# Performance work log

Hardware: AMD Instinct MI355X
Metric: run time of the kernel (lower is better)

## Reference

```python
import jax, jax.numpy as jnp
import numpy as np

VERY_NEG = -1e30

H = 768           # hidden_size
A_DIM = 768       # attention_dim_size
N_TREE = 40000    # num_tree_nodes (embed_init vocab)
N_CODES = 10000   # number of leaf codes (rows of leaves_list)
MAX_ANC = 8       # max ancestors per code
B, V, M = 16, 32, 48  # batch, visits, codes per visit
OUT = 512         # classifier output_size


def setup_inputs() -> dict:
    key = jax.random.key(0)
    ks = jax.random.split(key, 12)
    leaves_list = jax.random.randint(ks[0], (N_CODES, MAX_ANC), 0, N_TREE)
    ancestors_list = jax.random.randint(ks[1], (N_CODES, MAX_ANC), 0, N_TREE)
    masks = (jax.random.uniform(ks[2], (N_CODES, MAX_ANC)) > 0.3).astype(jnp.float32)
    masks = masks.at[:, 0].set(1.0)  # ensure at least one valid ancestor
    input_ids = jax.random.randint(ks[3], (B, V, M), 0, N_CODES + 1)  # 0 is padding row
    code_mask = (jax.random.uniform(ks[4], (B, V, M)) > 0.2).astype(jnp.float32)
    code_mask = code_mask.at[:, :, 0].set(1.0)
    s = 1.0 / np.sqrt(H)
    embed_table = jax.random.normal(ks[5], (N_TREE, H), dtype=jnp.float32) * s
    w1 = jax.random.normal(ks[6], (2 * H, A_DIM), dtype=jnp.float32) * (1.0 / np.sqrt(2 * H))
    b1 = jnp.zeros((A_DIM,), dtype=jnp.float32)
    w2 = jax.random.normal(ks[7], (A_DIM, 1), dtype=jnp.float32) * (1.0 / np.sqrt(A_DIM))
    b2 = jnp.zeros((1,), dtype=jnp.float32)
    wc = jax.random.normal(ks[8], (H, OUT), dtype=jnp.float32) * s
    bc = jnp.zeros((OUT,), dtype=jnp.float32)
    return {
        "embed_table": embed_table, "w1": w1, "b1": b1, "w2": w2, "b2": b2,
        "wc": wc, "bc": bc, "masks": masks, "code_mask": code_mask,
        "leaves_list": leaves_list, "ancestors_list": ancestors_list,
        "input_ids": input_ids,
    }


def reference(embed_table, w1, b1, w2, b2, wc, bc, masks, code_mask,
              leaves_list, ancestors_list, input_ids):
    # --- DAGAttention2D over ancestor axis ---
    leaves = embed_table[leaves_list]        # [N, A, H]
    ancestors = embed_table[ancestors_list]  # [N, A, H]
    m = masks[:, :, None]                    # [N, A, 1]
    x = jnp.concatenate([leaves * m, ancestors * m], axis=-1)  # [N, A, 2H]
    x = jax.nn.relu(jnp.einsum('nah,hd->nad', x, w1) + b1)
    x = jnp.einsum('nad,do->nao', x, w2) + b2                  # [N, A, 1]
    x = x + (1.0 - m) * VERY_NEG
    attn = jax.nn.softmax(x, axis=1)                           # softmax over ancestors
    dag_emb = (attn * ancestors * m).sum(axis=1)               # [N, H]
    # --- dict_matrix with padding row 0, embedding lookup ---
    dict_matrix = jnp.concatenate([jnp.zeros((1, dag_emb.shape[1]), dag_emb.dtype), dag_emb], axis=0)
    emb = dict_matrix[input_ids]             # [B, V, M, H]
    cm = code_mask[..., None]
    pooled = (emb * cm).sum(axis=2) / jnp.clip(cm.sum(axis=2), 1.0, None)  # [B, V, H]
    # --- Classifier (dropout inactive at eval, activation=None) ---
    out = jnp.einsum('bvh,ho->bvo', pooled, wc) + bc           # [B, V, OUT]
    return out
```

## Files before the change

### kernel.cpp

```cpp
#include <hip/hip_runtime.h>
#include <stdint.h>

typedef unsigned short u16;
typedef __bf16 bfx8 __attribute__((ext_vector_type(8)));
typedef float f32x4 __attribute__((ext_vector_type(4)));

#define HD 768
#define NTREE 40000
#define NCODES 10000
#define GNN 1536
#define OUTD 512
#define NBV 512
#define VNEG (-1e30f)
#define TB 4

#define BM 256
#define BN 256
#define BK 64
#define NKT (HD / BK)
#define NMT ((NTREE + BM - 1) / BM)
#define NNT (GNN / BN)
#define GRID (NMT * NNT)
#define Q8 (GRID / 8)
#define R8 (GRID % 8)

#define WAITV(n) asm volatile("s_waitcnt vmcnt(" #n ")" ::: "memory")
#define LGKM(n)  asm volatile("s_waitcnt lgkmcnt(" #n ")" ::: "memory")

__device__ __forceinline__ float bf2f(u16 u) {
  union { uint32_t i; float f; } v; v.i = ((uint32_t)u) << 16; return v.f;
}
__device__ __forceinline__ u16 f2bf(float f) {
  union { float fl; uint32_t i; } v; v.fl = f;
  uint32_t u = v.i;
  u += 0x7FFFu + ((u >> 16) & 1u);
  return (u16)(u >> 16);
}

#define NBLK_CONV 30000
__global__ void k_prep(const float* __restrict__ E, u16* __restrict__ Ebf,
                       const float* __restrict__ w1, u16* __restrict__ Bt) {
  const int bid = blockIdx.x, tid = threadIdx.x;
  if (bid < NBLK_CONV) {
    const int i = bid * 256 + tid;
    float4 v = ((const float4*)E)[i];
    ushort4 r;
    r.x = f2bf(v.x); r.y = f2bf(v.y); r.z = f2bf(v.z); r.w = f2bf(v.w);
    ((ushort4*)Ebf)[i] = r;
  } else {
    const int idx = (bid - NBLK_CONV) * 256 + tid;
    if (idx < GNN * HD) {
      const int n = idx / HD, k = idx % HD;
      const int srow = k + ((n >= HD) ? HD : 0);
      const int scol = (n >= HD) ? (n - HD) : n;
      Bt[idx] = f2bf(w1[(size_t)srow * HD + scol]);
    }
  }
}

__global__ __launch_bounds__(512, 2) void k_gemm(const u16* __restrict__ A,
                                                 const u16* __restrict__ B,
                                                 u16* __restrict__ C) {
  __shared__ u16 lds[65536];

  const int tid    = threadIdx.x;
  const int lane   = tid & 63;
  const int wv     = tid >> 6;
  const int wr     = wv >> 2;
  const int wc     = wv & 3;
  const int lane15 = lane & 15;
  const int g      = lane >> 4;

  const int orig = blockIdx.x;
  const int xcd = orig & 7, lin = orig >> 3;
  const int wg = (xcd < R8 ? xcd * (Q8 + 1) : R8 * (Q8 + 1) + (xcd - R8) * Q8) + lin;
  const int mt = wg / NNT, nt = wg % NNT;
  const int tm = mt * BM, tn = nt * BN;

  uint32_t aOff[2][2], bOff[2][2];
#pragma unroll
  for (int u = 0; u < 2; ++u) {
    const int o    = u * 8192 + tid * 16;
    const int rloc = o >> 7;
    const int c    = ((o >> 4) & 7) ^ (rloc & 7);
#pragma unroll
    for (int h = 0; h < 2; ++h) {
      int ra = tm + h * 128 + rloc; if (ra > NTREE - 1) ra = NTREE - 1;
      aOff[u][h] = (uint32_t)ra * HD + c * 8;
      bOff[u][h] = (uint32_t)(tn + h * 128 + rloc) * HD + c * 8;
    }
  }

#define STAGE_A(MH, NB, TT) do {                                               \
    _Pragma("unroll") for (int u = 0; u < 2; ++u)                              \
      __builtin_amdgcn_global_load_lds(                                        \
        (const __attribute__((address_space(1))) void*)(A + aOff[u][MH] + (TT) * BK), \
        (__attribute__((address_space(3))) void*)((char*)lds + (NB) * 32768 +  \
            (MH) * 16384 + u * 8192 + tid * 16),                               \
        16, 0, 0);                                                             \
  } while (0)

#define STAGE_B(NH, NB, TT) do {                                               \
    _Pragma("unroll") for (int u = 0; u < 2; ++u)                              \
      __builtin_amdgcn_global_load_lds(                                        \
        (const __attribute__((address_space(1))) void*)(B + bOff[u][NH] + (TT) * BK), \
        (__attribute__((address_space(3))) void*)((char*)lds + 65536 +         \
            (NB) * 32768 + (NH) * 16384 + u * 8192 + tid * 16),                \
        16, 0, 0);                                                             \
  } while (0)

  f32x4 acc[4][4][2];
#pragma unroll
  for (int q = 0; q < 4; ++q)
#pragma unroll
    for (int i = 0; i < 4; ++i)
#pragma unroll
      for (int j = 0; j < 2; ++j) acc[q][i][j] = (f32x4){0.f, 0.f, 0.f, 0.f};

  int colz[2];
  colz[0] = ((0 * 4 + g) ^ (lane15 & 7)) * 8;
  colz[1] = ((1 * 4 + g) ^ (lane15 & 7)) * 8;
  const int aLane = wr * 4096 + lane15 * 64;
  const int bLane = wc * 2048 + lane15 * 64;

  bfx8 aF[4][2], bF[2][2];

#define READ_A(MH, BA) do {                                                    \
    _Pragma("unroll") for (int mf = 0; mf < 4; ++mf)                           \
      _Pragma("unroll") for (int ks = 0; ks < 2; ++ks)                         \
        aF[mf][ks] = *(const bfx8*)&lds[(BA) + (MH) * 8192 + aLane +           \
                                        mf * 1024 + colz[ks]];                 \
  } while (0)

#define READ_B(NH, BB) do {                                                    \
    _Pragma("unroll") for (int nf = 0; nf < 2; ++nf)                           \
      _Pragma("unroll") for (int ks = 0; ks < 2; ++ks)                         \
        bF[nf][ks] = *(const bfx8*)&lds[(BB) + (NH) * 8192 + bLane +           \
                                        nf * 1024 + colz[ks]];                 \
  } while (0)

#define MFMA_Q(Q) do {                                                         \
    LGKM(0);                                                                   \
    __builtin_amdgcn_sched_barrier(0);                                         \
    __builtin_amdgcn_s_setprio(1);                                             \
    _Pragma("unroll") for (int mf = 0; mf < 4; ++mf)                           \
      _Pragma("unroll") for (int nf = 0; nf < 2; ++nf)                         \
        _Pragma("unroll") for (int ks = 0; ks < 2; ++ks)                       \
          acc[Q][mf][nf] = __builtin_amdgcn_mfma_f32_16x16x32_bf16(            \
              aF[mf][ks], bF[nf][ks], acc[Q][mf][nf], 0, 0, 0);                \
    __builtin_amdgcn_s_setprio(0);                                             \
  } while (0)

  STAGE_A(0, 0, 0);
  STAGE_B(0, 0, 0);
  STAGE_B(1, 0, 0);
  STAGE_A(1, 0, 0);
  WAITV(4);
  __builtin_amdgcn_s_barrier();

  for (int t = 0; t < NKT; ++t) {
    const int bA = (t & 1) * 16384;
    const int bB = 32768 + (t & 1) * 16384;
    const int nb = (t + 1) & 1;
    const bool more = (t + 1 < NKT);

    READ_A(0, bA);
    READ_B(0, bB);
    if (more) STAGE_A(0, nb, t + 1);
    MFMA_Q(0);
    if (more) { WAITV(4); } else { WAITV(2); }
    __builtin_amdgcn_s_barrier();

    READ_B(1, bB);
    if (more) STAGE_B(0, nb, t + 1);
    MFMA_Q(1);
    if (more) { WAITV(4); } else { WAITV(0); }
    __builtin_amdgcn_s_barrier();

    READ_A(1, bA);
    if (more) STAGE_B(1, nb, t + 1);
    MFMA_Q(2);
    __builtin_amdgcn_s_barrier();

    READ_B(0, bB);
    if (more) STAGE_A(1, nb, t + 1);
    MFMA_Q(3);
    if (more) { WAITV(4); }
    __builtin_amdgcn_s_barrier();
  }

  const int r0 = (lane >> 4) * 4, cc = lane15;
  const int qmh[4] = {0, 0, 1, 1}, qnh[4] = {0, 1, 1, 0};
#pragma unroll
  for (int q = 0; q < 4; ++q) {
#pragma unroll
    for (int mf = 0; mf < 4; ++mf) {
#pragma unroll
      for (int nf = 0; nf < 2; ++nf) {
#pragma unroll
        for (int rr = 0; rr < 4; ++rr) {
          const int row = tm + qmh[q] * 128 + wr * 64 + mf * 16 + r0 + rr;
          if (row < NTREE) {
            const int col = tn + qnh[q] * 128 + wc * 32 + nf * 16 + cc;
            C[(size_t)row * GNN + col] = f2bf(acc[q][mf][nf][rr]);
          }
        }
      }
    }
  }
#undef MFMA_Q
#undef READ_A
#undef READ_B
#undef STAGE_A
#undef STAGE_B
}

__global__ __launch_bounds__(512) void k_attn(const u16* __restrict__ PQ,
                                              const u16* __restrict__ Ebf,
                                              const float* __restrict__ b1,
                                              const float* __restrict__ w2,
                                              const float* __restrict__ b2,
                                              const float* __restrict__ masks,
                                              const int* __restrict__ leaves,
                                              const int* __restrict__ anc,
                                              u16* __restrict__ dag) {
  const int n = blockIdx.x;
  const int tid = threadIdx.x, lane = tid & 63, wv = tid >> 6;
  __shared__ float sc[8];
  __shared__ float m_s[8];
  __shared__ int   an_s[8];
  __shared__ int   lv_s[8];
  if (tid < 8) {
    an_s[tid] = anc[n * 8 + tid];
    lv_s[tid] = leaves[n * 8 + tid];
    m_s[tid]  = masks[n * 8 + tid];
  }
  __syncthreads();

  {
    const int a = wv;
    const float mm = m_s[a];
    if (mm == 0.f) {
      if (lane == 0) sc[a] = VNEG;
    } else {
      const int l = lv_s[a], an = an_s[a];
      const u16* pr = PQ + (size_t)l * GNN;
      const u16* qr = PQ + (size_t)an * GNN + HD;
      const int d0 = lane * 12;
      float s = 0.f;
#pragma unroll
      for (int jj = 0; jj < 3; ++jj) {
        const int d = d0 + jj * 4;
        ushort4 pv = *(const ushort4*)(pr + d);
        ushort4 qv = *(const ushort4*)(qr + d);
        float4  bb = *(const float4*)(b1 + d);
        float4  ww = *(const float4*)(w2 + d);
        float v;
        v = fmaxf(bf2f(pv.x) + bf2f(qv.x) + bb.x, 0.f); s += v * ww.x;
        v = fmaxf(bf2f(pv.y) + bf2f(qv.y) + bb.y, 0.f); s += v * ww.y;
        v = fmaxf(bf2f(pv.z) + bf2f(qv.z) + bb.z, 0.f); s += v * ww.z;
        v = fmaxf(bf2f(pv.w) + bf2f(qv.w) + bb.w, 0.f); s += v * ww.w;
      }
#pragma unroll
      for (int off = 32; off > 0; off >>= 1) s += __shfl_down(s, off);
      if (lane == 0) sc[a] = s + b2[0];
    }
  }
  __syncthreads();

  float mx = sc[0];
#pragma unroll
  for (int a = 1; a < 8; ++a) mx = fmaxf(mx, sc[a]);
  float ex[8], den = 0.f;
#pragma unroll
  for (int a = 0; a < 8; ++a) { ex[a] = expf(sc[a] - mx); den += ex[a]; }
  const float inv = 1.0f / den;
  float cf[8];
#pragma unroll
  for (int a = 0; a < 8; ++a) cf[a] = ex[a] * inv * m_s[a];

  if (tid < 384) {
    const int d = tid * 2;
    float a0 = 0.f, a1 = 0.f;
#pragma unroll
    for (int a = 0; a < 8; ++a) {
      const float cfa = cf[a];
      if (cfa != 0.f) {
        const uint32_t w = *(const uint32_t*)(Ebf + (size_t)an_s[a] * HD + d);
        a0 += cfa * bf2f((u16)(w & 0xffffu));
        a1 += cfa * bf2f((u16)(w >> 16));
      }
    }
    const uint32_t packed = (uint32_t)f2bf(a0) | ((uint32_t)f2bf(a1) << 16);
    *(uint32_t*)(dag + (size_t)n * HD + d) = packed;
  }
}

__global__ __launch_bounds__(256) void k_pool(const u16* __restrict__ dag,
                                              const int* __restrict__ ids,
                                              const float* __restrict__ cm,
                                              float* __restrict__ pooled) {
  const int bv = blockIdx.x, tid = threadIdx.x;
  __shared__ int   id_s[48];
  __shared__ float cm_s[48];
  if (tid < 48) { id_s[tid] = ids[bv * 48 + tid]; cm_s[tid] = cm[bv * 48 + tid]; }
  __syncthreads();
  float cnt = 0.f;
  for (int m = 0; m < 48; ++m) cnt += cm_s[m];
  const float scale = 1.0f / fmaxf(cnt, 1.0f);
  if (tid < 192) {
    float4 accv = make_float4(0.f, 0.f, 0.f, 0.f);
    for (int m = 0; m < 48; ++m) {
      const int id = id_s[m];
      const float cv = cm_s[m];
      if (id > 0 && cv != 0.f) {
        ushort4 v = *(const ushort4*)(dag + (size_t)(id - 1) * HD + tid * 4);
        accv.x += cv * bf2f(v.x); accv.y += cv * bf2f(v.y);
        accv.z += cv * bf2f(v.z); accv.w += cv * bf2f(v.w);
      }
    }
    accv.x *= scale; accv.y *= scale; accv.z *= scale; accv.w *= scale;
    *(float4*)(pooled + (size_t)bv * HD + tid * 4) = accv;
  }
}

__global__ __launch_bounds__(256) void k_out(const float* __restrict__ pooled,
                                             const float* __restrict__ wc,
                                             const float* __restrict__ bc,
                                             float* __restrict__ out) {
  const int b0 = blockIdx.x * TB;
  const int tid = threadIdx.x;
  __shared__ float pl[TB][HD];
  for (int i = tid; i < TB * HD; i += 256) pl[i / HD][i % HD] = pooled[(size_t)b0 * HD + i];
  __syncthreads();
  float a0[TB], a1[TB];
#pragma unroll
  for (int r = 0; r < TB; ++r) { a0[r] = 0.f; a1[r] = 0.f; }
  for (int h = 0; h < HD; ++h) {
    const float w0  = wc[(size_t)h * OUTD + tid];
    const float w1v = wc[(size_t)h * OUTD + tid + 256];
#pragma unroll
    for (int r = 0; r < TB; ++r) { const float p = pl[r][h]; a0[r] += p * w0; a1[r] += p * w1v; }
  }
  const float bc0 = bc[tid], bc1 = bc[tid + 256];
#pragma unroll
  for (int r = 0; r < TB; ++r) {
    out[(size_t)(b0 + r) * OUTD + tid]       = a0[r] + bc0;
    out[(size_t)(b0 + r) * OUTD + tid + 256] = a1[r] + bc1;
  }
}

extern "C" void kernel_launch(void* const* d_in, const int* in_sizes, int n_in,
                              void* d_out, int out_size, void* d_ws, size_t ws_size,
                              hipStream_t stream) {
  const float* E     = (const float*)d_in[0];
  const float* w1    = (const float*)d_in[1];
  const float* b1    = (const float*)d_in[2];
  const float* w2    = (const float*)d_in[3];
  const float* b2    = (const float*)d_in[4];
  const float* wc    = (const float*)d_in[5];
  const float* bc    = (const float*)d_in[6];
  const float* masks = (const float*)d_in[7];
  const float* cm    = (const float*)d_in[8];
  const int*   leaves = (const int*)d_in[9];
  const int*   anc    = (const int*)d_in[10];
  const int*   ids    = (const int*)d_in[11];
  float* out = (float*)d_out;

  if (n_in < 12) return;
  if (in_sizes[0] != NTREE * HD) return;
  if (out_size != NBV * OUTD) return;

  char* ws = (char*)d_ws;
  const size_t szEbf = (size_t)NTREE * HD * 2;
  const size_t szBt  = (size_t)GNN * HD * 2;
  const size_t szPQ  = (size_t)NTREE * GNN * 2;
  const size_t szDag = (size_t)NCODES * HD * 2;
  const size_t szPl  = (size_t)NBV * HD * 4;
  if (ws_size < szEbf + szBt + szPQ + szDag + szPl) return;

  u16*   Ebf    = (u16*)ws;            ws += szEbf;
  u16*   Bt     = (u16*)ws;            ws += szBt;
  u16*   PQ     = (u16*)ws;            ws += szPQ;
  u16*   dag    = (u16*)ws;            ws += szDag;
  float* pooled = (float*)ws;          ws += szPl;

  const int nPrep = NBLK_CONV + (GNN * HD + 255) / 256;
  k_prep<<<nPrep, 256, 0, stream>>>(E, Ebf, w1, Bt);
  k_gemm<<<GRID, 512, 0, stream>>>(Ebf, Bt, PQ);
  k_attn<<<NCODES, 512, 0, stream>>>(PQ, Ebf, b1, w2, b2, masks, leaves, anc, dag);
  k_pool<<<NBV, 256, 0, stream>>>(dag, ids, cm, pooled);
  k_out<<<NBV / TB, 256, 0, stream>>>(pooled, wc, bc, out);
}
```

Before: 277.0 us.

## Keep both B fragment halves in registers and restructure GEMM phase barriers

```diff
diff --git a/kernel.cpp b/kernel.cpp
--- a/kernel.cpp
+++ b/kernel.cpp
@@ -12,7 +12,7 @@
 #define OUTD 512
 #define NBV 512
 #define VNEG (-1e30f)
-#define TB 4
+#define TB 8
 
 #define BM 256
 #define BN 256
@@ -25,7 +25,6 @@
 #define R8 (GRID % 8)
 
 #define WAITV(n) asm volatile("s_waitcnt vmcnt(" #n ")" ::: "memory")
-#define LGKM(n)  asm volatile("s_waitcnt lgkmcnt(" #n ")" ::: "memory")
 
 __device__ __forceinline__ float bf2f(u16 u) {
   union { uint32_t i; float f; } v; v.i = ((uint32_t)u) << 16; return v.f;
@@ -123,7 +122,9 @@
   const int aLane = wr * 4096 + lane15 * 64;
   const int bLane = wc * 2048 + lane15 * 64;
 
-  bfx8 aF[4][2], bF[2][2];
+  bfx8 aF[4][2];
+  bfx8 bN0[2][2];
+  bfx8 bN1[2][2];
 
 #define READ_A(MH, BA) do {                                                    \
     _Pragma("unroll") for (int mf = 0; mf < 4; ++mf)                           \
@@ -132,22 +133,20 @@
                                         mf * 1024 + colz[ks]];                 \
   } while (0)
 
-#define READ_B(NH, BB) do {                                                    \
+#define READ_B(DST, NH, BB) do {                                               \
     _Pragma("unroll") for (int nf = 0; nf < 2; ++nf)                           \
       _Pragma("unroll") for (int ks = 0; ks < 2; ++ks)                         \
-        bF[nf][ks] = *(const bfx8*)&lds[(BB) + (NH) * 8192 + bLane +           \
-                                        nf * 1024 + colz[ks]];                 \
-  } while (0)
-
-#define MFMA_Q(Q) do {                                                         \
-    LGKM(0);                                                                   \
-    __builtin_amdgcn_sched_barrier(0);                                         \
+        DST[nf][ks] = *(const bfx8*)&lds[(BB) + (NH) * 8192 + bLane +          \
+                                         nf * 1024 + colz[ks]];                \
+  } while (0)
+
+#define MFMA_Q(Q, BFR) do {                                                    \
     __builtin_amdgcn_s_setprio(1);                                             \
     _Pragma("unroll") for (int mf = 0; mf < 4; ++mf)                           \
       _Pragma("unroll") for (int nf = 0; nf < 2; ++nf)                         \
         _Pragma("unroll") for (int ks = 0; ks < 2; ++ks)                       \
           acc[Q][mf][nf] = __builtin_amdgcn_mfma_f32_16x16x32_bf16(            \
-              aF[mf][ks], bF[nf][ks], acc[Q][mf][nf], 0, 0, 0);                \
+              aF[mf][ks], BFR[nf][ks], acc[Q][mf][nf], 0, 0, 0);               \
     __builtin_amdgcn_s_setprio(0);                                             \
   } while (0)
 
@@ -165,26 +164,29 @@
     const bool more = (t + 1 < NKT);
 
     READ_A(0, bA);
-    READ_B(0, bB);
+    READ_B(bN0, 0, bB);
     if (more) STAGE_A(0, nb, t + 1);
-    MFMA_Q(0);
+    __builtin_amdgcn_s_barrier();
+    MFMA_Q(0, bN0);
     if (more) { WAITV(4); } else { WAITV(2); }
     __builtin_amdgcn_s_barrier();
 
-    READ_B(1, bB);
+    READ_B(bN1, 1, bB);
     if (more) STAGE_B(0, nb, t + 1);
-    MFMA_Q(1);
+    __builtin_amdgcn_s_barrier();
+    MFMA_Q(1, bN1);
     if (more) { WAITV(4); } else { WAITV(0); }
     __builtin_amdgcn_s_barrier();
 
     READ_A(1, bA);
     if (more) STAGE_B(1, nb, t + 1);
-    MFMA_Q(2);
-    __builtin_amdgcn_s_barrier();
-
-    READ_B(0, bB);
+    __builtin_amdgcn_s_barrier();
+    MFMA_Q(2, bN1);
+    __builtin_amdgcn_s_barrier();
+
     if (more) STAGE_A(1, nb, t + 1);
-    MFMA_Q(3);
+    __builtin_amdgcn_s_barrier();
+    MFMA_Q(3, bN0);
     if (more) { WAITV(4); }
     __builtin_amdgcn_s_barrier();
   }
```

Measured after the change: 297.0 us. 1.07x slower.
